# Kernel tuning notes

Hardware: AMD Instinct MI355X
Metric: run time of the kernel (lower is better)

Reference implementation:

```python
import jax, jax.numpy as jnp
import numpy as np

IMAGE_SIZE = (224, 224)
SIGMA = 4.0
KS = 2 * int(4.0 * SIGMA + 0.5) + 1  # 33


def _gaussian_kernel2d(ks, sigma):
    x = jnp.arange(ks, dtype=jnp.float32) - (ks - 1) / 2.0
    g = jnp.exp(-(x ** 2) / (2.0 * sigma ** 2))
    g = g / g.sum()
    return jnp.outer(g, g)  # already sums to 1; normalize_kernel2d is a no-op


def setup_inputs() -> dict:
    key = jax.random.key(0)
    k1, k2, k3 = jax.random.split(key, 3)
    B, C, H, W = 32, 200, 56, 56
    HW = H * W
    embedding = jax.random.normal(k1, (B, C, H, W), dtype=jnp.float32)
    mean = jax.random.normal(k2, (C, HW), dtype=jnp.float32)
    A = jax.random.normal(k3, (HW, C, C), dtype=jnp.float32)
    # PSD per-pixel inverse covariance, as produced by real PaDiM statistics
    inv_covariance = jnp.einsum('nij,nkj->nik', A, A) / C + 0.1 * jnp.eye(C, dtype=jnp.float32)
    covariance = jnp.zeros((1,), dtype=jnp.float32)  # unused on mahalanobis path
    return {"embedding": embedding, "mean": mean,
            "inv_covariance": inv_covariance, "covariance": covariance}


def reference(embedding, mean, inv_covariance, covariance):
    B, C, H, W = embedding.shape
    HW = H * W
    emb = embedding.reshape(B, C, HW)
    # delta: [HW, B, C]
    delta = jnp.transpose(emb - mean[None], (2, 0, 1))
    # per-pixel mahalanobis quadratic form: diag(delta @ inv_cov @ delta^T)
    md = jnp.matmul(delta, inv_covariance)          # [HW, B, C]
    q = jnp.sum(md * delta, axis=-1)                # [HW, B]
    dist = jnp.sqrt(jnp.clip(q, 0.0, None))
    score = jnp.transpose(dist, (1, 0)).reshape(B, 1, H, W)
    # bilinear upsample (align_corners=False == half-pixel centers)
    up = jax.image.resize(score, (B, 1, IMAGE_SIZE[0], IMAGE_SIZE[1]), method='bilinear')
    # gaussian blur, reflect 'same' padding, single channel
    kernel = _gaussian_kernel2d(KS, SIGMA)[None, None]  # [1,1,KS,KS]
    pad = (KS - 1) // 2
    padded = jnp.pad(up, ((0, 0), (0, 0), (pad, pad), (pad, pad)), mode='reflect')
    out = jax.lax.conv_general_dilated(padded, kernel, window_strides=(1, 1),
                                       padding='VALID')
    return out
```

## Files before the change

kernel.cpp:

```cpp
#include <hip/hip_runtime.h>
#include <math.h>

#define HW   3136
#define NC   200
#define NB   32
#define SS   56
#define OS   224
#define KS   33
#define GPAD 16

typedef __attribute__((ext_vector_type(8))) short          short8;
typedef __attribute__((ext_vector_type(4))) float          f32x4;
typedef __attribute__((ext_vector_type(4))) unsigned short ush4;

__device__ __forceinline__ unsigned short f2bf(float x) {
    unsigned int u = __builtin_bit_cast(unsigned int, x);
    u += 0x7FFFu + ((u >> 16) & 1u);
    return (unsigned short)(u >> 16);
}
__device__ __forceinline__ float bf2f(unsigned short h) {
    unsigned int u = ((unsigned int)h) << 16;
    return __builtin_bit_cast(float, u);
}

__device__ __forceinline__ void gload16(const void* g, void* l) {
    __builtin_amdgcn_global_load_lds(
        (const __attribute__((address_space(1))) void*)g,
        (__attribute__((address_space(3))) void*)l, 16, 0, 0);
}

__global__ __launch_bounds__(256)
void k_delta(const float* __restrict__ emb,
             const float* __restrict__ mean,
             unsigned short* __restrict__ dg) {
    const int tile = blockIdx.x >> 2;
    const int bq   = blockIdx.x & 3;
    const int n0   = tile * 16;
    const int t    = threadIdx.x;

    __shared__ float          mm[32 * 20];
    __shared__ unsigned short tr[256 * 20];

    unsigned int* dgU = (unsigned int*)dg;

    for (int kt = 0; kt < 7; kt++) {
        const int c0 = kt * 32;
        if (t < 128) {
            int cl = t >> 2, nl4 = (t & 3) * 4;
            int c = c0 + cl;
            float4 v = {0.f, 0.f, 0.f, 0.f};
            if (c < NC) v = *(const float4*)&mean[(size_t)c * HW + n0 + nl4];
            *(float4*)&mm[cl * 20 + nl4] = v;
        }
        __syncthreads();
#pragma unroll
        for (int j = 0; j < 4; j++) {
            int row = (t >> 2) + 64 * j;
            int nl4 = (t & 3) * 4;
            int b   = bq * 8 + (row >> 5);
            int cl  = row & 31;
            int c   = c0 + cl;
            ush4 wv = {0, 0, 0, 0};
            if (c < NC) {
                float4 e = *(const float4*)&emb[((size_t)(b * NC + c)) * HW + n0 + nl4];
                float4 m = *(const float4*)&mm[cl * 20 + nl4];
                wv[0] = f2bf(e.x - m.x); wv[1] = f2bf(e.y - m.y);
                wv[2] = f2bf(e.z - m.z); wv[3] = f2bf(e.w - m.w);
            }
            *(ush4*)&tr[row * 20 + nl4] = wv;
        }
        __syncthreads();
#pragma unroll
        for (int j = 0; j < 8; j++) {
            int idx = t + 256 * j;
            int nl  = idx >> 7, rem = idx & 127;
            int bl  = rem >> 4, cu = rem & 15;
            int cb  = bl * 32 + 2 * cu;
            unsigned int lo = tr[cb * 20 + nl];
            unsigned int hi = tr[(cb + 1) * 20 + nl];
            dgU[((size_t)(n0 + nl) * 7 + kt) * 512 +
                (size_t)(bq * 8 + bl) * 16 + cu] = lo | (hi << 16);
        }
        __syncthreads();
    }
}

__global__ __launch_bounds__(256, 4)
void k_mahal2(const unsigned short* __restrict__ dg,
              const float* __restrict__ icov,
              float* __restrict__ score) {
    const int bid = blockIdx.x;
    const int n = (bid & 7) * 392 + (bid >> 3);
    const int t = threadIdx.x;

    __shared__ __align__(16) unsigned short dd[7 * 1024];
    __shared__ __align__(16) float slab[2][3200];
    __shared__ float qs[NB];

    const float* Mn   = icov + (size_t)n * (NC * NC);
    const char*  dsrc = (const char*)(dg + (size_t)n * 7168);

    {
        char* lb = (char*)dd;
#pragma unroll
        for (int i = 0; i < 4; i++) {
            int idx = i * 256 + t;
            if (idx < 896)
                gload16(dsrc + (size_t)idx * 16, lb + (i * 256 + (t & 192)) * 16);
        }
        const char* ms = (const char*)Mn;
        char* sb = (char*)&slab[0][0];
        if (t < 88) {
            int row = t / 5;
            int c   = t - row * 5;
            if (row >= 16) { row = 15; c = 0; }
            if (c >= 4) c = 0;
            gload16(ms + (size_t)row * (NC * 4) + (size_t)c * 16,
                    sb + (t & 192) * 16);
        }
    }
    if (t < NB) qs[t] = 0.f;
    __syncthreads();

    const int lane = t & 63;
    const int w    = t >> 6;
    const int col  = lane & 15;
    const int quad = lane >> 4;
    const int bt   = w & 1;
    const int kg   = w >> 1;
    const int ddb  = (bt * 16 + col) * 32;

    short8 bF[4];
#pragma unroll
    for (int q = 0; q < 4; q++) {
        int kt = kg + 2 * q;
        if (kt < 7)
            bF[q] = *(const short8*)&dd[kt * 1024 + ddb + quad * 8];
    }

    float qacc = 0.f;

#pragma unroll
    for (int it = 0; it < 13; it++) {
        if (it < 12) {
            const int tt  = it + 1;
            const int nr  = (tt == 12) ? 8 : 16;
            const int CHn = (4 * (tt + 1) < 50) ? 4 * (tt + 1) : 50;
            const int CHpn = CHn + 1;
            const int T   = nr * CHpn + 8;
            const char* ms = (const char*)(Mn + (size_t)tt * 16 * NC);
            char* sb = (char*)&slab[tt & 1][0];
#pragma unroll
            for (int i = 0; i < 4; i++) {
                int idx = i * 256 + t;
                if (idx < T) {
                    int row = idx / CHpn;
                    int c   = idx - row * CHpn;
                    if (row >= nr) { row = nr - 1; c = 0; }
                    if (c >= CHn) c = 0;
                    gload16(ms + (size_t)row * (NC * 4) + (size_t)c * 16,
                            sb + (i * 256 + (t & 192)) * 16);
                }
            }
        }
        {
            const int CH   = (4 * (it + 1) < 50) ? 4 * (it + 1) : 50;
            const int strd = (CH + 1) * 4;
            const int Cq   = (it + 2) >> 1;
            const int ig   = 16 * it + col;
            const float* sl = &slab[it & 1][0];
            f32x4 acc = {0.f, 0.f, 0.f, 0.f};
#pragma unroll
            for (int q = 0; q < 4; q++) {
                const int cq = kg + 2 * q;
                if (cq < Cq) {
                    const int half0 = 32 * cq + (quad >> 1) * 16;
                    float s = 0.f;
                    if (ig < NC) {
                        if (half0 + 16 <= 16 * it) s = 2.f;
                        else if (half0 == 16 * it) s = 1.f;
                    }
                    short8 aF = {0, 0, 0, 0, 0, 0, 0, 0};
                    if (s != 0.f) {
                        const f32x4* ap =
                            (const f32x4*)&sl[col * strd + cq * 32 + quad * 8];
                        f32x4 lo = ap[0], hi = ap[1];
                        aF[0] = f2bf(s * lo[0]); aF[1] = f2bf(s * lo[1]);
                        aF[2] = f2bf(s * lo[2]); aF[3] = f2bf(s * lo[3]);
                        aF[4] = f2bf(s * hi[0]); aF[5] = f2bf(s * hi[1]);
                        aF[6] = f2bf(s * hi[2]); aF[7] = f2bf(s * hi[3]);
                    }
                    acc = __builtin_amdgcn_mfma_f32_16x16x32_bf16(aF, bF[q], acc, 0, 0, 0);
                }
            }
            int off = (it >> 1) * 1024 + ddb + (it & 1) * 16 + quad * 4;
            ush4 dv = *(const ush4*)&dd[off];
            float v = acc[0] * bf2f(dv[0]) + acc[1] * bf2f(dv[1]) +
                      acc[2] * bf2f(dv[2]) + acc[3] * bf2f(dv[3]);
            v += __shfl_xor(v, 16);
            v += __shfl_xor(v, 32);
            qacc += v;
        }
        __syncthreads();
    }

    if (quad == 0) atomicAdd(&qs[bt * 16 + col], qacc);
    __syncthreads();
    if (t < NB) {
        float q = qs[t];
        score[(size_t)t * HW + n] = sqrtf(q > 0.f ? q : 0.f);
    }
}

__global__ void k_upsample(const float* __restrict__ score,
                           float* __restrict__ up) {
    int idx = blockIdx.x * 256 + threadIdx.x;
    if (idx >= NB * OS * OS) return;
    int x = idx % OS;
    int y = (idx / OS) % OS;
    int b = idx / (OS * OS);

    float sy = 0.25f * y - 0.375f;
    float sx = 0.25f * x - 0.375f;
    int y0 = (int)floorf(sy); float fy = sy - (float)y0;
    int x0 = (int)floorf(sx); float fx = sx - (float)x0;
    int y0c = min(max(y0, 0), SS - 1), y1c = min(max(y0 + 1, 0), SS - 1);
    int x0c = min(max(x0, 0), SS - 1), x1c = min(max(x0 + 1, 0), SS - 1);

    const float* sb = score + (size_t)b * HW;
    float v00 = sb[y0c * SS + x0c];
    float v01 = sb[y0c * SS + x1c];
    float v10 = sb[y1c * SS + x0c];
    float v11 = sb[y1c * SS + x1c];
    up[idx] = (1.f - fy) * ((1.f - fx) * v00 + fx * v01) +
              fy * ((1.f - fx) * v10 + fx * v11);
}

__global__ void k_gauss_init(float* __restrict__ g) {
    if (threadIdx.x == 0) {
        float e[KS];
        float sum = 0.f;
        for (int i = 0; i < KS; i++) {
            float x = (float)i - 16.0f;
            e[i] = expf(-(x * x) / 32.0f);
            sum += e[i];
        }
        for (int i = 0; i < KS; i++) g[i] = e[i] / sum;
    }
}

__device__ __forceinline__ int reflect224(int i) {
    if (i < 0) return -i;
    if (i > OS - 1) return 2 * (OS - 1) - i;
    return i;
}

__global__ void k_hblur(const float* __restrict__ up,
                        const float* __restrict__ g,
                        float* __restrict__ tmp) {
    int idx = blockIdx.x * 256 + threadIdx.x;
    if (idx >= NB * OS * OS) return;
    int x = idx % OS;
    int row = idx / OS;
    const float* src = up + (size_t)row * OS;
    float acc = 0.f;
#pragma unroll
    for (int t = -GPAD; t <= GPAD; t++) {
        acc += g[t + GPAD] * src[reflect224(x + t)];
    }
    tmp[idx] = acc;
}

__global__ void k_vblur(const float* __restrict__ tmp,
                        const float* __restrict__ g,
                        float* __restrict__ out) {
    int idx = blockIdx.x * 256 + threadIdx.x;
    if (idx >= NB * OS * OS) return;
    int x = idx % OS;
    int y = (idx / OS) % OS;
    int b = idx / (OS * OS);
    const float* src = tmp + (size_t)b * OS * OS;
    float acc = 0.f;
#pragma unroll
    for (int t = -GPAD; t <= GPAD; t++) {
        acc += g[t + GPAD] * src[(size_t)reflect224(y + t) * OS + x];
    }
    out[idx] = acc;
}

extern "C" void kernel_launch(void* const* d_in, const int* in_sizes, int n_in,
                              void* d_out, int out_size, void* d_ws, size_t ws_size,
                              hipStream_t stream) {
    const float* emb  = (const float*)d_in[0];
    const float* mean = (const float*)d_in[1];
    const float* icov = (const float*)d_in[2];
    float* out = (float*)d_out;

    char* ws = (char*)d_ws;
    float* g     = (float*)ws;
    float* score = (float*)(ws + 256);
    float* tmp   = (float*)(ws + 256 + 401408);
    unsigned short* dg = (unsigned short*)(ws + 6824192);

    const int up_blocks = (NB * OS * OS) / 256;

    k_gauss_init<<<1, 64, 0, stream>>>(g);
    k_delta<<<784, 256, 0, stream>>>(emb, mean, dg);
    k_mahal2<<<HW, 256, 0, stream>>>(dg, icov, score);
    k_upsample<<<up_blocks, 256, 0, stream>>>(score, out);
    k_hblur<<<up_blocks, 256, 0, stream>>>(out, g, tmp);
    k_vblur<<<up_blocks, 256, 0, stream>>>(tmp, g, out);
}
```

Measured before the change: 720.1 us.

## Fold bilinear upsample and separable Gaussian blur into precomputed 224x56 matrices

Replaces the upsample, horizontal blur and vertical blur kernels with one fused post-processing kernel. Upsampling with reflect padding followed by a separable blur is linear, so it is expressed as W·S·Wᵀ, with a 224x56 composite weight matrix W built on device. Each block stages a strip of the 56x56 score map in shared memory, applies Wᵀ along columns, then W along rows for 32 output rows. This removes two full-resolution intermediate buffers and their global-memory round trips, at the cost of a small weight-building kernel and per-block redundant column work.

```diff
diff --git a/kernel.cpp b/kernel.cpp
--- a/kernel.cpp
+++ b/kernel.cpp
@@ -7,7 +7,6 @@
 #define SS   56
 #define OS   224
 #define KS   33
-#define GPAD 16
 
 typedef __attribute__((ext_vector_type(8))) short          short8;
 typedef __attribute__((ext_vector_type(4))) float          f32x4;
@@ -212,80 +211,85 @@
     }
 }
 
-__global__ void k_upsample(const float* __restrict__ score,
-                           float* __restrict__ up) {
+__global__ __launch_bounds__(256)
+void k_winit(float* __restrict__ W, float* __restrict__ WT) {
     int idx = blockIdx.x * 256 + threadIdx.x;
-    if (idx >= NB * OS * OS) return;
-    int x = idx % OS;
-    int y = (idx / OS) % OS;
-    int b = idx / (OS * OS);
-
-    float sy = 0.25f * y - 0.375f;
-    float sx = 0.25f * x - 0.375f;
-    int y0 = (int)floorf(sy); float fy = sy - (float)y0;
-    int x0 = (int)floorf(sx); float fx = sx - (float)x0;
-    int y0c = min(max(y0, 0), SS - 1), y1c = min(max(y0 + 1, 0), SS - 1);
-    int x0c = min(max(x0, 0), SS - 1), x1c = min(max(x0 + 1, 0), SS - 1);
-
+    if (idx >= 224 * 64) return;
+    int y = idx >> 6, r = idx & 63;
+
+    float e[KS]; float sum = 0.f;
+#pragma unroll
+    for (int i = 0; i < KS; i++) {
+        float xx = (float)i - 16.0f;
+        e[i] = expf(-(xx * xx) / 32.0f);
+        sum += e[i];
+    }
+    float w = 0.f;
+    if (r < 56) {
+#pragma unroll
+        for (int tt = 0; tt < KS; tt++) {
+            int i = y + tt - 16;
+            if (i < 0) i = -i;
+            if (i > OS - 1) i = 2 * (OS - 1) - i;
+            float si = 0.25f * (float)i - 0.375f;
+            int r0 = (int)floorf(si);
+            float f = si - (float)r0;
+            int r0c = min(max(r0, 0), SS - 1);
+            int r1c = min(max(r0 + 1, 0), SS - 1);
+            float u = ((r == r0c) ? (1.f - f) : 0.f) + ((r == r1c) ? f : 0.f);
+            w += (e[tt] / sum) * u;
+        }
+    }
+    W[y * 64 + r] = w;
+    if (r < 56) WT[r * 224 + y] = w;
+}
+
+__global__ __launch_bounds__(256)
+void k_post(const float* __restrict__ score,
+            const float* __restrict__ W,
+            const float* __restrict__ WT,
+            float* __restrict__ out) {
+    const int b  = blockIdx.x / 7;
+    const int yt = blockIdx.x % 7;
+    const int y0 = yt * 32;
+    const int t  = threadIdx.x;
+
+    const int imin = max(0, y0 - 16);
+    const int imax = min(OS - 1, y0 + 47);
+    const int rlo  = max(0, (int)floorf(0.25f * (float)imin - 0.375f));
+    const int rhi  = min(SS, (int)floorf(0.25f * (float)imax - 0.375f) + 2);
+    const int NR   = rhi - rlo;
+
+    __shared__ float S[20 * 60];
     const float* sb = score + (size_t)b * HW;
-    float v00 = sb[y0c * SS + x0c];
-    float v01 = sb[y0c * SS + x1c];
-    float v10 = sb[y1c * SS + x0c];
-    float v11 = sb[y1c * SS + x1c];
-    up[idx] = (1.f - fy) * ((1.f - fx) * v00 + fx * v01) +
-              fy * ((1.f - fx) * v10 + fx * v11);
-}
-
-__global__ void k_gauss_init(float* __restrict__ g) {
-    if (threadIdx.x == 0) {
-        float e[KS];
-        float sum = 0.f;
-        for (int i = 0; i < KS; i++) {
-            float x = (float)i - 16.0f;
-            e[i] = expf(-(x * x) / 32.0f);
-            sum += e[i];
-        }
-        for (int i = 0; i < KS; i++) g[i] = e[i] / sum;
-    }
-}
-
-__device__ __forceinline__ int reflect224(int i) {
-    if (i < 0) return -i;
-    if (i > OS - 1) return 2 * (OS - 1) - i;
-    return i;
-}
-
-__global__ void k_hblur(const float* __restrict__ up,
-                        const float* __restrict__ g,
-                        float* __restrict__ tmp) {
-    int idx = blockIdx.x * 256 + threadIdx.x;
-    if (idx >= NB * OS * OS) return;
-    int x = idx % OS;
-    int row = idx / OS;
-    const float* src = up + (size_t)row * OS;
-    float acc = 0.f;
-#pragma unroll
-    for (int t = -GPAD; t <= GPAD; t++) {
-        acc += g[t + GPAD] * src[reflect224(x + t)];
-    }
-    tmp[idx] = acc;
-}
-
-__global__ void k_vblur(const float* __restrict__ tmp,
-                        const float* __restrict__ g,
-                        float* __restrict__ out) {
-    int idx = blockIdx.x * 256 + threadIdx.x;
-    if (idx >= NB * OS * OS) return;
-    int x = idx % OS;
-    int y = (idx / OS) % OS;
-    int b = idx / (OS * OS);
-    const float* src = tmp + (size_t)b * OS * OS;
-    float acc = 0.f;
-#pragma unroll
-    for (int t = -GPAD; t <= GPAD; t++) {
-        acc += g[t + GPAD] * src[(size_t)reflect224(y + t) * OS + x];
-    }
-    out[idx] = acc;
+    for (int idx = t; idx < 20 * 14; idx += 256) {
+        int j = idx / 14, c4 = (idx % 14) * 4;
+        float4 v = {0.f, 0.f, 0.f, 0.f};
+        if (j < NR) v = *(const float4*)&sb[(rlo + j) * SS + c4];
+        *(float4*)&S[j * 60 + c4] = v;
+    }
+    __syncthreads();
+
+    if (t < OS) {
+        const int x = t;
+        float T[20];
+#pragma unroll
+        for (int j = 0; j < 20; j++) T[j] = 0.f;
+        for (int c = 0; c < SS; c++) {
+            float wv = WT[c * OS + x];
+#pragma unroll
+            for (int j = 0; j < 20; j++) T[j] += S[j * 60 + c] * wv;
+        }
+        float* ob = out + (size_t)b * (OS * OS);
+#pragma unroll 4
+        for (int y = y0; y < y0 + 32; y++) {
+            const float* wr = W + (size_t)y * 64 + rlo;
+            float acc = 0.f;
+#pragma unroll
+            for (int j = 0; j < 20; j++) acc += wr[j] * T[j];
+            ob[(size_t)y * OS + x] = acc;
+        }
+    }
 }
 
 extern "C" void kernel_launch(void* const* d_in, const int* in_sizes, int n_in,
@@ -297,17 +301,13 @@
     float* out = (float*)d_out;
 
     char* ws = (char*)d_ws;
-    float* g     = (float*)ws;
     float* score = (float*)(ws + 256);
-    float* tmp   = (float*)(ws + 256 + 401408);
+    float* W     = (float*)(ws + 401664);
+    float* WT    = (float*)(ws + 459008);
     unsigned short* dg = (unsigned short*)(ws + 6824192);
 
-    const int up_blocks = (NB * OS * OS) / 256;
-
-    k_gauss_init<<<1, 64, 0, stream>>>(g);
+    k_winit<<<56, 256, 0, stream>>>(W, WT);
     k_delta<<<784, 256, 0, stream>>>(emb, mean, dg);
     k_mahal2<<<HW, 256, 0, stream>>>(dg, icov, score);
-    k_upsample<<<up_blocks, 256, 0, stream>>>(score, out);
-    k_hblur<<<up_blocks, 256, 0, stream>>>(out, g, tmp);
-    k_vblur<<<up_blocks, 256, 0, stream>>>(tmp, g, out);
-}
+    k_post<<<NB * 7, 256, 0, stream>>>(score, W, WT, out);
+}
```

Measured after the change: 712.0 us. About the same (-1.1%).
